# Kernel optimization log

Measured on AMD Instinct MI355X. Metric: run time of the kernel, lower is better.

Reference implementation:

```python
import jax, jax.numpy as jnp
import numpy as np

N = 50000      # nodes
E = 800000     # edges (avg degree 16)
C = 5000       # clusters (Kongming compression)
D = 128        # in_features
OUT = 40       # out_features (classes)
K = 2          # propagation hops


def setup_inputs() -> dict:
    key = jax.random.key(0)
    k1, k2, k3, k4, k5, k6 = jax.random.split(key, 6)
    x = jax.random.normal(k1, (N, D), dtype=jnp.float32)
    edge_index = jax.random.randint(k2, (2, E), 0, N, dtype=jnp.int32)
    cluster_index = jax.random.randint(k3, (N,), 0, C, dtype=jnp.int32)
    rep_idx = jax.random.randint(k4, (C,), 0, N, dtype=jnp.int32)
    W = jax.random.normal(k5, (OUT, D), dtype=jnp.float32) / np.sqrt(D)
    b = jax.random.normal(k6, (OUT,), dtype=jnp.float32) * 0.01
    return {"x": x, "edge_index": edge_index, "cluster_index": cluster_index,
            "rep_idx": rep_idx, "W": W, "b": b}


def _gcn_propagate(x, edge_index, k_hops):
    # PUPropagate: K hops of D^{-1/2}(A+I)D^{-1/2} x (gcn_norm with self-loops)
    n = x.shape[0]
    loops = jnp.arange(n, dtype=edge_index.dtype)
    src = jnp.concatenate([edge_index[0], loops])
    dst = jnp.concatenate([edge_index[1], loops])
    deg = jax.ops.segment_sum(jnp.ones_like(src, dtype=x.dtype), dst, num_segments=n)
    dinv = jnp.where(deg > 0, jax.lax.rsqrt(deg), 0.0)
    norm = (dinv[src] * dinv[dst])[:, None]            # [E+N, 1]
    h = x
    for _ in range(k_hops):                            # small fixed hop count
        h = jax.ops.segment_sum(h[src] * norm, dst, num_segments=n)
    return h


def reference(x, edge_index, cluster_index, rep_idx, W, b):
    h = _gcn_propagate(x, edge_index, K)               # [N, D]
    # Kongming_Cluster: gather one representative row per cluster
    hc = h[rep_idx]                                    # [C, D]
    yc = hc @ W.T + b                                  # [C, OUT] dense linear on compressed rows
    # Kongming_Reconstruct: scatter back to all nodes by cluster index
    y = yc[cluster_index]                              # [N, OUT]
    return jax.nn.log_softmax(y, axis=1)
```

## Files before the change

### kernel.cpp

```cpp
#include <hip/hip_runtime.h>
#include <math.h>

#define N_NODES 50000
#define N_EDGES 800000
#define N_CLUST 5000
#define DIM     128
#define NOUT    40
#define SLOTS   64

#define FILL_PART   8
#define NODES_PER_P (N_NODES / FILL_PART)
#define FILL_CHUNKS 100
#define EPC (N_EDGES / FILL_CHUNKS)

typedef __attribute__((ext_vector_type(8))) short short8;
typedef __attribute__((ext_vector_type(4))) float fvec4;

__device__ __forceinline__ short bf16r(float v) {
    unsigned u = __float_as_uint(v);
    u = (u + 0x7FFFu + ((u >> 16) & 1u)) >> 16;
    return (short)u;
}
__device__ __forceinline__ unsigned pack_bf16x2(float a, float b) {
    unsigned ua = __float_as_uint(a);
    unsigned ub = __float_as_uint(b);
    ua = (ua + 0x7FFFu + ((ua >> 16) & 1u)) >> 16;
    ub = (ub + 0x7FFFu + ((ub >> 16) & 1u)) >> 16;
    return ua | (ub << 16);
}
__device__ __forceinline__ float2 unpack_bf16x2(unsigned v) {
    float2 r;
    r.x = __uint_as_float(v << 16);
    r.y = __uint_as_float(v & 0xFFFF0000u);
    return r;
}

__global__ __launch_bounds__(256) void fill_slots(const int4* __restrict__ src4,
                                                  const int4* __restrict__ dst4,
                                                  int* __restrict__ cnt,
                                                  unsigned short* __restrict__ slot) {
    int p = blockIdx.x & (FILL_PART - 1);
    int chunk = blockIdx.x >> 3;
    int lo = p * NODES_PER_P;
    int hi = lo + NODES_PER_P;
    int q0 = chunk * (EPC / 4);
    #pragma unroll 2
    for (int i = threadIdx.x; i < EPC / 4; i += 256) {
        int4 d4 = dst4[q0 + i];
        if (d4.x >= lo && d4.x < hi) {
            int s = ((const int*)src4)[(q0 + i) * 4 + 0];
            int pos = atomicAdd(&cnt[d4.x], 1);
            if (pos < SLOTS) slot[d4.x * SLOTS + pos] = (unsigned short)s;
        }
        if (d4.y >= lo && d4.y < hi) {
            int s = ((const int*)src4)[(q0 + i) * 4 + 1];
            int pos = atomicAdd(&cnt[d4.y], 1);
            if (pos < SLOTS) slot[d4.y * SLOTS + pos] = (unsigned short)s;
        }
        if (d4.z >= lo && d4.z < hi) {
            int s = ((const int*)src4)[(q0 + i) * 4 + 2];
            int pos = atomicAdd(&cnt[d4.z], 1);
            if (pos < SLOTS) slot[d4.z * SLOTS + pos] = (unsigned short)s;
        }
        if (d4.w >= lo && d4.w < hi) {
            int s = ((const int*)src4)[(q0 + i) * 4 + 3];
            int pos = atomicAdd(&cnt[d4.w], 1);
            if (pos < SLOTS) slot[d4.w * SLOTS + pos] = (unsigned short)s;
        }
    }
}

__global__ __launch_bounds__(256) void zgemm(const float* __restrict__ x,
                                             const float* __restrict__ W,
                                             const int* __restrict__ cnt,
                                             unsigned short* __restrict__ zs) {
    int lane = threadIdx.x & 63;
    int wv = threadIdx.x >> 6;
    int q = lane >> 4, r16 = lane & 15;
    int tile = blockIdx.x * 4 + wv;
    if (tile >= N_NODES / 16) return;

    short8 bf[3][4];
    #pragma unroll
    for (int t = 0; t < 3; t++) {
        int o = t * 16 + r16;
        #pragma unroll
        for (int s = 0; s < 4; s++) {
            short8 f = {0, 0, 0, 0, 0, 0, 0, 0};
            if (o < NOUT) {
                const float* wp = W + o * DIM + s * 32 + q * 8;
                float4 w0 = *(const float4*)wp;
                float4 w1 = *(const float4*)(wp + 4);
                f[0] = bf16r(w0.x); f[1] = bf16r(w0.y);
                f[2] = bf16r(w0.z); f[3] = bf16r(w0.w);
                f[4] = bf16r(w1.x); f[5] = bf16r(w1.y);
                f[6] = bf16r(w1.z); f[7] = bf16r(w1.w);
            }
            bf[t][s] = f;
        }
    }

    int node = tile * 16 + r16;
    float dn = rsqrtf((float)cnt[node] + 1.0f);
    short8 af[4];
    #pragma unroll
    for (int s = 0; s < 4; s++) {
        const float* xp = x + (size_t)node * DIM + s * 32 + q * 8;
        float4 a0 = *(const float4*)xp;
        float4 a1 = *(const float4*)(xp + 4);
        short8 f;
        f[0] = bf16r(dn * a0.x); f[1] = bf16r(dn * a0.y);
        f[2] = bf16r(dn * a0.z); f[3] = bf16r(dn * a0.w);
        f[4] = bf16r(dn * a1.x); f[5] = bf16r(dn * a1.y);
        f[6] = bf16r(dn * a1.z); f[7] = bf16r(dn * a1.w);
        af[s] = f;
    }

    fvec4 acc0 = {0, 0, 0, 0}, acc1 = {0, 0, 0, 0}, acc2 = {0, 0, 0, 0};
    #pragma unroll
    for (int s = 0; s < 4; s++) {
        acc0 = __builtin_amdgcn_mfma_f32_16x16x32_bf16(af[s], bf[0][s], acc0, 0, 0, 0);
        acc1 = __builtin_amdgcn_mfma_f32_16x16x32_bf16(af[s], bf[1][s], acc1, 0, 0, 0);
        acc2 = __builtin_amdgcn_mfma_f32_16x16x32_bf16(af[s], bf[2][s], acc2, 0, 0, 0);
    }

    #pragma unroll
    for (int r = 0; r < 4; r++) {
        int nd = tile * 16 + q * 4 + r;
        unsigned short* zrow = zs + (size_t)nd * NOUT;
        zrow[r16]      = (unsigned short)bf16r(acc0[r]);
        zrow[16 + r16] = (unsigned short)bf16r(acc1[r]);
        if (r16 < 8) zrow[32 + r16] = (unsigned short)bf16r(acc2[r]);
    }
}

__global__ __launch_bounds__(256) void hop_all(const unsigned* __restrict__ zs,
                                               unsigned* __restrict__ v1,
                                               const unsigned short* __restrict__ slot,
                                               const int* __restrict__ cnt) {
    int lane = threadIdx.x & 63;
    int g = lane / 20;
    int k = lane - g * 20;
    int wv = threadIdx.x >> 6;
    int n = blockIdx.x * 12 + wv * 3 + g;
    if (g >= 3 || n >= N_NODES) return;
    int c = cnt[n];
    int m = (c < SLOTS) ? c : SLOTS;
    float s = 1.0f / (float)(c + 1);
    float2 accA = unpack_bf16x2(zs[n * 20 + k]);
    float2 accB; accB.x = 0.0f; accB.y = 0.0f;
    int base = n * SLOTS;
    int j = 0;
    for (; j + 3 < m; j += 4) {
        unsigned ss0 = *(const unsigned*)&slot[base + j];
        unsigned ss1 = *(const unsigned*)&slot[base + j + 2];
        float2 f0 = unpack_bf16x2(zs[(int)(ss0 & 0xFFFFu) * 20 + k]);
        float2 f1 = unpack_bf16x2(zs[(int)(ss0 >> 16) * 20 + k]);
        float2 f2 = unpack_bf16x2(zs[(int)(ss1 & 0xFFFFu) * 20 + k]);
        float2 f3 = unpack_bf16x2(zs[(int)(ss1 >> 16) * 20 + k]);
        accA.x += f0.x + f1.x;
        accA.y += f0.y + f1.y;
        accB.x += f2.x + f3.x;
        accB.y += f2.y + f3.y;
    }
    for (; j < m; j++) {
        float2 f0 = unpack_bf16x2(zs[(int)slot[base + j] * 20 + k]);
        accB.x += f0.x; accB.y += f0.y;
    }
    v1[n * 20 + k] = pack_bf16x2(s * (accA.x + accB.x), s * (accA.y + accB.y));
}

__global__ __launch_bounds__(256) void rep_lsm(const unsigned* __restrict__ v1,
                                               const unsigned short* __restrict__ slot,
                                               const int* __restrict__ cnt,
                                               const int* __restrict__ rep_idx,
                                               const float2* __restrict__ b2,
                                               float2* __restrict__ yc2) {
    int lane = threadIdx.x & 63;
    int wv = threadIdx.x >> 6;
    int c = blockIdx.x * 4 + wv;
    if (c >= N_CLUST) return;
    int n = rep_idx[c];
    int cn = cnt[n];
    int m = (cn < SLOTS) ? cn : SLOTS;
    float dn = rsqrtf((float)(cn + 1));
    int g = lane / 20;
    int k = lane - g * 20;
    float2 acc; acc.x = 0.0f; acc.y = 0.0f;
    if (g == 0) acc = unpack_bf16x2(v1[n * 20 + k]);
    if (g < 3) {
        int base = n * SLOTS;
        for (int j = g; j < m; j += 3) {
            float2 f = unpack_bf16x2(v1[(int)slot[base + j] * 20 + k]);
            acc.x += f.x; acc.y += f.y;
        }
    }
    float t1x = __shfl(acc.x, lane + 20), t1y = __shfl(acc.y, lane + 20);
    float t2x = __shfl(acc.x, lane + 40), t2y = __shfl(acc.y, lane + 40);
    bool act = (lane < 20);
    float2 h; h.x = 0.0f; h.y = 0.0f;
    if (act) {
        float2 bb = b2[k];
        h.x = dn * (acc.x + t1x + t2x) + bb.x;
        h.y = dn * (acc.y + t1y + t2y) + bb.y;
    }
    float mx = act ? fmaxf(h.x, h.y) : -INFINITY;
    #pragma unroll
    for (int off = 32; off; off >>= 1) mx = fmaxf(mx, __shfl_xor(mx, off));
    float e = act ? (expf(h.x - mx) + expf(h.y - mx)) : 0.0f;
    #pragma unroll
    for (int off = 32; off; off >>= 1) e += __shfl_xor(e, off);
    float lg = mx + logf(e);
    if (act) {
        float2 o; o.x = h.x - lg; o.y = h.y - lg;
        yc2[(size_t)c * 20 + k] = o;
    }
}

__global__ void gather_out(const float4* __restrict__ yc4, const int* __restrict__ cidx,
                           float4* __restrict__ out4) {
    int t = blockIdx.x * blockDim.x + threadIdx.x;
    if (t >= N_NODES * (NOUT / 4)) return;
    int n = t / (NOUT / 4);
    int q = t - n * (NOUT / 4);
    out4[t] = yc4[(size_t)cidx[n] * (NOUT / 4) + q];
}

extern "C" void kernel_launch(void* const* d_in, const int* in_sizes, int n_in,
                              void* d_out, int out_size, void* d_ws, size_t ws_size,
                              hipStream_t stream) {
    const float* x    = (const float*)d_in[0];
    const int*   esrc = (const int*)d_in[1];
    const int*   edst = ((const int*)d_in[1]) + N_EDGES;
    const int*   cidx = (const int*)d_in[2];
    const int*   ridx = (const int*)d_in[3];
    const float* W    = (const float*)d_in[4];
    const float* b    = (const float*)d_in[5];
    float* out = (float*)d_out;

    char* ws = (char*)d_ws;
    size_t off = 0;
    auto alloc = [&](size_t bytes) { char* p = ws + off; off += (bytes + 255) & ~size_t(255); return p; };
    int*            cnt  = (int*)alloc(N_NODES * 4);
    unsigned short* slot = (unsigned short*)alloc((size_t)N_NODES * SLOTS * 2);
    unsigned short* zs   = (unsigned short*)alloc((size_t)N_NODES * NOUT * 2);
    unsigned*       v1   = (unsigned*)alloc((size_t)N_NODES * (NOUT / 2) * 4);
    float*          yc   = (float*)alloc((size_t)N_CLUST * NOUT * 4);
    (void)ws_size; (void)in_sizes; (void)n_in; (void)out_size;

    hipMemsetAsync(cnt, 0, N_NODES * 4, stream);

    const int B = 256;
    fill_slots<<<FILL_PART * FILL_CHUNKS, 256, 0, stream>>>((const int4*)esrc,
                                                            (const int4*)edst, cnt, slot);
    zgemm<<<(N_NODES / 16 + 3) / 4, 256, 0, stream>>>(x, W, cnt, zs);
    hop_all<<<(N_NODES + 11) / 12, 256, 0, stream>>>((const unsigned*)zs, v1, slot, cnt);
    rep_lsm<<<(N_CLUST + 3) / 4, 256, 0, stream>>>(v1, slot, cnt, ridx,
                                                   (const float2*)b, (float2*)yc);
    int gt = N_NODES * (NOUT / 4);
    gather_out<<<(gt + B - 1) / B, B, 0, stream>>>((const float4*)yc, cidx, (float4*)out);
}
```

Measured before the change: 166.4 us.

## XCC-aware persistent work queue for slot fill and wider hop gathers

fill_slots becomes a persistent kernel of 512 blocks. Each block reads its XCC id from a hardware register and claims (partition, chunk) work items from per-partition atomic counters, preferring the partition that matches its XCC. The aim is to keep the atomics for each node range on one XCC's L2. The edge source indices are now read as int4 vectors instead of scalar loads. hop_all gathers 8-byte bf16x4 values per lane and handles 6 nodes per wave instead of 3, which halves the number of gather instructions per row but adds more register work per lane.

```diff
diff --git a/kernel.cpp b/kernel.cpp
--- a/kernel.cpp
+++ b/kernel.cpp
@@ -12,6 +12,7 @@
 #define NODES_PER_P (N_NODES / FILL_PART)
 #define FILL_CHUNKS 100
 #define EPC (N_EDGES / FILL_CHUNKS)
+#define HWREG_XCC_ID ((31 << 11) | (0 << 6) | 20)
 
 typedef __attribute__((ext_vector_type(8))) short short8;
 typedef __attribute__((ext_vector_type(4))) float fvec4;
@@ -34,38 +35,58 @@
     r.y = __uint_as_float(v & 0xFFFF0000u);
     return r;
 }
+__device__ __forceinline__ float4 unpack_bf16x4(uint2 v) {
+    float4 r;
+    r.x = __uint_as_float(v.x << 16);
+    r.y = __uint_as_float(v.x & 0xFFFF0000u);
+    r.z = __uint_as_float(v.y << 16);
+    r.w = __uint_as_float(v.y & 0xFFFF0000u);
+    return r;
+}
 
 __global__ __launch_bounds__(256) void fill_slots(const int4* __restrict__ src4,
                                                   const int4* __restrict__ dst4,
                                                   int* __restrict__ cnt,
-                                                  unsigned short* __restrict__ slot) {
-    int p = blockIdx.x & (FILL_PART - 1);
-    int chunk = blockIdx.x >> 3;
-    int lo = p * NODES_PER_P;
-    int hi = lo + NODES_PER_P;
-    int q0 = chunk * (EPC / 4);
-    #pragma unroll 2
-    for (int i = threadIdx.x; i < EPC / 4; i += 256) {
-        int4 d4 = dst4[q0 + i];
-        if (d4.x >= lo && d4.x < hi) {
-            int s = ((const int*)src4)[(q0 + i) * 4 + 0];
-            int pos = atomicAdd(&cnt[d4.x], 1);
-            if (pos < SLOTS) slot[d4.x * SLOTS + pos] = (unsigned short)s;
-        }
-        if (d4.y >= lo && d4.y < hi) {
-            int s = ((const int*)src4)[(q0 + i) * 4 + 1];
-            int pos = atomicAdd(&cnt[d4.y], 1);
-            if (pos < SLOTS) slot[d4.y * SLOTS + pos] = (unsigned short)s;
-        }
-        if (d4.z >= lo && d4.z < hi) {
-            int s = ((const int*)src4)[(q0 + i) * 4 + 2];
-            int pos = atomicAdd(&cnt[d4.z], 1);
-            if (pos < SLOTS) slot[d4.z * SLOTS + pos] = (unsigned short)s;
-        }
-        if (d4.w >= lo && d4.w < hi) {
-            int s = ((const int*)src4)[(q0 + i) * 4 + 3];
-            int pos = atomicAdd(&cnt[d4.w], 1);
-            if (pos < SLOTS) slot[d4.w * SLOTS + pos] = (unsigned short)s;
+                                                  unsigned short* __restrict__ slot,
+                                                  int* __restrict__ pctr) {
+    __shared__ int s_p, s_c;
+    for (;;) {
+        if (threadIdx.x == 0) {
+            int xcc = (int)(__builtin_amdgcn_s_getreg(HWREG_XCC_ID) & 7u);
+            int p = -1, c = -1;
+            for (int t = 0; t < FILL_PART; t++) {
+                int pp = (xcc + t) & (FILL_PART - 1);
+                int cc = atomicAdd(&pctr[pp], 1);
+                if (cc < FILL_CHUNKS) { p = pp; c = cc; break; }
+            }
+            s_p = p; s_c = c;
+        }
+        __syncthreads();
+        int p = s_p, chunk = s_c;
+        __syncthreads();
+        if (chunk < 0) return;
+        int lo = p * NODES_PER_P;
+        int hi = lo + NODES_PER_P;
+        int q0 = chunk * (EPC / 4);
+        for (int i = threadIdx.x; i < EPC / 4; i += 256) {
+            int4 d4 = dst4[q0 + i];
+            int4 s4 = src4[q0 + i];
+            if (d4.x >= lo && d4.x < hi) {
+                int pos = atomicAdd(&cnt[d4.x], 1);
+                if (pos < SLOTS) slot[d4.x * SLOTS + pos] = (unsigned short)s4.x;
+            }
+            if (d4.y >= lo && d4.y < hi) {
+                int pos = atomicAdd(&cnt[d4.y], 1);
+                if (pos < SLOTS) slot[d4.y * SLOTS + pos] = (unsigned short)s4.y;
+            }
+            if (d4.z >= lo && d4.z < hi) {
+                int pos = atomicAdd(&cnt[d4.z], 1);
+                if (pos < SLOTS) slot[d4.z * SLOTS + pos] = (unsigned short)s4.z;
+            }
+            if (d4.w >= lo && d4.w < hi) {
+                int pos = atomicAdd(&cnt[d4.w], 1);
+                if (pos < SLOTS) slot[d4.w * SLOTS + pos] = (unsigned short)s4.w;
+            }
         }
     }
 }
@@ -134,40 +155,43 @@
     }
 }
 
-__global__ __launch_bounds__(256) void hop_all(const unsigned* __restrict__ zs,
-                                               unsigned* __restrict__ v1,
+__global__ __launch_bounds__(256) void hop_all(const uint2* __restrict__ zs2,
+                                               uint2* __restrict__ v12,
                                                const unsigned short* __restrict__ slot,
                                                const int* __restrict__ cnt) {
     int lane = threadIdx.x & 63;
-    int g = lane / 20;
-    int k = lane - g * 20;
+    int g = lane / 10;
+    int k = lane - g * 10;
     int wv = threadIdx.x >> 6;
-    int n = blockIdx.x * 12 + wv * 3 + g;
-    if (g >= 3 || n >= N_NODES) return;
+    int n = blockIdx.x * 24 + wv * 6 + g;
+    if (g >= 6 || n >= N_NODES) return;
     int c = cnt[n];
     int m = (c < SLOTS) ? c : SLOTS;
     float s = 1.0f / (float)(c + 1);
-    float2 accA = unpack_bf16x2(zs[n * 20 + k]);
-    float2 accB; accB.x = 0.0f; accB.y = 0.0f;
+    float4 accA = unpack_bf16x4(zs2[n * 10 + k]);
+    float4 accB; accB.x = accB.y = accB.z = accB.w = 0.0f;
     int base = n * SLOTS;
     int j = 0;
     for (; j + 3 < m; j += 4) {
         unsigned ss0 = *(const unsigned*)&slot[base + j];
         unsigned ss1 = *(const unsigned*)&slot[base + j + 2];
-        float2 f0 = unpack_bf16x2(zs[(int)(ss0 & 0xFFFFu) * 20 + k]);
-        float2 f1 = unpack_bf16x2(zs[(int)(ss0 >> 16) * 20 + k]);
-        float2 f2 = unpack_bf16x2(zs[(int)(ss1 & 0xFFFFu) * 20 + k]);
-        float2 f3 = unpack_bf16x2(zs[(int)(ss1 >> 16) * 20 + k]);
-        accA.x += f0.x + f1.x;
-        accA.y += f0.y + f1.y;
-        accB.x += f2.x + f3.x;
-        accB.y += f2.y + f3.y;
+        float4 f0 = unpack_bf16x4(zs2[(int)(ss0 & 0xFFFFu) * 10 + k]);
+        float4 f1 = unpack_bf16x4(zs2[(int)(ss0 >> 16) * 10 + k]);
+        float4 f2 = unpack_bf16x4(zs2[(int)(ss1 & 0xFFFFu) * 10 + k]);
+        float4 f3 = unpack_bf16x4(zs2[(int)(ss1 >> 16) * 10 + k]);
+        accA.x += f0.x + f1.x;  accA.y += f0.y + f1.y;
+        accA.z += f0.z + f1.z;  accA.w += f0.w + f1.w;
+        accB.x += f2.x + f3.x;  accB.y += f2.y + f3.y;
+        accB.z += f2.z + f3.z;  accB.w += f2.w + f3.w;
     }
     for (; j < m; j++) {
-        float2 f0 = unpack_bf16x2(zs[(int)slot[base + j] * 20 + k]);
-        accB.x += f0.x; accB.y += f0.y;
-    }
-    v1[n * 20 + k] = pack_bf16x2(s * (accA.x + accB.x), s * (accA.y + accB.y));
+        float4 f0 = unpack_bf16x4(zs2[(int)slot[base + j] * 10 + k]);
+        accB.x += f0.x; accB.y += f0.y; accB.z += f0.z; accB.w += f0.w;
+    }
+    uint2 p;
+    p.x = pack_bf16x2(s * (accA.x + accB.x), s * (accA.y + accB.y));
+    p.y = pack_bf16x2(s * (accA.z + accB.z), s * (accA.w + accB.w));
+    v12[n * 10 + k] = p;
 }
 
 __global__ __launch_bounds__(256) void rep_lsm(const unsigned* __restrict__ v1,
@@ -241,21 +265,23 @@
     char* ws = (char*)d_ws;
     size_t off = 0;
     auto alloc = [&](size_t bytes) { char* p = ws + off; off += (bytes + 255) & ~size_t(255); return p; };
-    int*            cnt  = (int*)alloc(N_NODES * 4);
+    int*            cnt  = (int*)alloc((N_NODES + FILL_PART) * 4);
+    int*            pctr = cnt + N_NODES;
     unsigned short* slot = (unsigned short*)alloc((size_t)N_NODES * SLOTS * 2);
     unsigned short* zs   = (unsigned short*)alloc((size_t)N_NODES * NOUT * 2);
     unsigned*       v1   = (unsigned*)alloc((size_t)N_NODES * (NOUT / 2) * 4);
     float*          yc   = (float*)alloc((size_t)N_CLUST * NOUT * 4);
     (void)ws_size; (void)in_sizes; (void)n_in; (void)out_size;
 
-    hipMemsetAsync(cnt, 0, N_NODES * 4, stream);
+    hipMemsetAsync(cnt, 0, (N_NODES + FILL_PART) * 4, stream);
 
     const int B = 256;
-    fill_slots<<<FILL_PART * FILL_CHUNKS, 256, 0, stream>>>((const int4*)esrc,
-                                                            (const int4*)edst, cnt, slot);
+    fill_slots<<<512, 256, 0, stream>>>((const int4*)esrc, (const int4*)edst,
+                                        cnt, slot, pctr);
     zgemm<<<(N_NODES / 16 + 3) / 4, 256, 0, stream>>>(x, W, cnt, zs);
-    hop_all<<<(N_NODES + 11) / 12, 256, 0, stream>>>((const unsigned*)zs, v1, slot, cnt);
-    rep_lsm<<<(N_CLUST + 3) / 4, 256, 0, stream>>>(v1, slot, cnt, ridx,
+    hop_all<<<(N_NODES + 23) / 24, 256, 0, stream>>>((const uint2*)zs, (uint2*)v1,
+                                                     slot, cnt);
+    rep_lsm<<<(N_CLUST + 3) / 4, 256, 0, stream>>>((const unsigned*)v1, slot, cnt, ridx,
                                                    (const float2*)b, (float2*)yc);
     int gt = N_NODES * (NOUT / 4);
     gather_out<<<(gt + B - 1) / B, B, 0, stream>>>((const float4*)yc, cidx, (float4*)out);
```

New measurement: 203.0 us. 22.0% more time.
